# Optimization experiments

Hardware: AMD Instinct MI355X
Metric: run time of the kernel (lower is better)

Reference implementation:

```python
import jax, jax.numpy as jnp
import numpy as np

IN, H, OUT = 8, 256, 24  # input_size, hidden_size, output_size
B, T = 2048, 256


def _gate_step(hx, x, Wx, Wh, b):
    # Fused version of the 8 per-gate Linears: one [.,IN]@[IN,4H] + one [.,H]@[H,4H]
    gates = x @ Wx + hx @ Wh + b            # [B, 4H]
    i, f, o, g = jnp.split(gates, 4, axis=-1)
    i, f, o = jax.nn.sigmoid(i), jax.nn.sigmoid(f), jax.nn.sigmoid(o)
    g = jnp.tanh(g)
    # NOTE: in the original code cx is never reassigned, so it stays zeros and
    # cy = cx*f + i*g == i*g on every step. We replicate that exactly.
    cy = i * g
    return o * jnp.tanh(cy)


def setup_inputs() -> dict:
    key = jax.random.key(0)
    ks = jax.random.split(key, 9)
    s = 0.05
    return {
        "inputs0": jax.random.normal(ks[0], (B, T, IN), jnp.float32),
        "inputs1": jax.random.normal(ks[1], (B, OUT - 1), jnp.float32),
        # concatenated gate weights, order [i | f | o | c]
        "Wx": jax.random.normal(ks[2], (IN, 4 * H), jnp.float32) * s,
        "Wh": jax.random.normal(ks[3], (H, 4 * H), jnp.float32) * s,
        "b": jax.random.normal(ks[4], (4 * H,), jnp.float32) * s,  # bx + bh folded
        "Wy": jax.random.normal(ks[5], (H, 1), jnp.float32) * s,
        "by": jax.random.normal(ks[6], (1,), jnp.float32) * s,
        # fresh random Linear(1, IN) per decoder step in the original -> per-step params
        "dec_w": jax.random.normal(ks[7], (OUT - 1, IN), jnp.float32) * s,
        "dec_b": jax.random.normal(ks[8], (OUT - 1, IN), jnp.float32) * s,
    }


def reference(inputs0, inputs1, Wx, Wh, b, Wy, by, dec_w, dec_b):
    bsz = inputs0.shape[0]
    h0 = jnp.zeros((bsz, H), inputs0.dtype)

    # ---- encoder: scan over time (strict recurrence) ----
    x_seq = jnp.transpose(inputs0, (1, 0, 2))  # [T, B, IN]

    def enc_step(h, x):
        return _gate_step(h, x, Wx, Wh, b), None

    h, _ = jax.lax.scan(enc_step, h0, x_seq)
    hy0 = h @ Wy + by                           # [B, 1]

    # ---- decoder: OUT-1 steps, each with its own fresh 1->IN linear ----
    x1_seq = jnp.transpose(inputs1, (1, 0))[: OUT - 1]  # [OUT-1, B]

    def dec_step(h, inp):
        x1, w, bb = inp
        x = x1[:, None] * w[None, :] + bb[None, :]      # [B, IN]
        h = _gate_step(h, x, Wx, Wh, b)
        return h, h @ Wy + by                            # y: [B, 1]

    _, ys = jax.lax.scan(dec_step, h, (x1_seq, dec_w, dec_b))  # ys: [OUT-1, B, 1]

    hy = jnp.concatenate([hy0, jnp.transpose(ys[..., 0], (1, 0))], axis=1)  # [B, OUT]
    return hy
```

## Files before the change

### kernel.cpp

```cpp
#include <hip/hip_runtime.h>


typedef short bf16x8 __attribute__((ext_vector_type(8)));
typedef float f32x4 __attribute__((ext_vector_type(4)));

#define T_ENC 256
#define N_DEC 23
#define NSTEP 279
#define HSTR 296
#define REG_T 45
#define LDS_T 9
#define WPACK_SHORTS (48 * 9 * 512)

__device__ __forceinline__ short f2bf(float f) {
  unsigned u = __float_as_uint(f);
  u = (u + 0x7fffu + ((u >> 16) & 1u)) >> 16;
  return (short)u;
}
__device__ __forceinline__ float bf2f(short s) {
  return __uint_as_float(((unsigned)(unsigned short)s) << 16);
}

#if __has_builtin(__builtin_amdgcn_rcpf)
#define RCPF(x) __builtin_amdgcn_rcpf(x)
#else
#define RCPF(x) (1.0f / (x))
#endif

__device__ __forceinline__ float sigm(float x) { return RCPF(1.0f + __expf(-x)); }
__device__ __forceinline__ float tanhf_fast(float x) {
  return 1.0f - 2.0f * RCPF(__expf(2.0f * x) + 1.0f);
}

__global__ void pack_kernel(const float* __restrict__ Wx, const float* __restrict__ Wh,
                            const float* __restrict__ b, short* __restrict__ Wpack) {
  int tau = blockIdx.x;
  int l = threadIdx.x;
  int n_tile = tau / 9, kt = tau % 9;
  int w = n_tile / 6, t = n_tile % 6;
  int gate = t >> 1, loc = t & 1;
  int base = (gate == 0) ? 0 : (gate == 1 ? 512 : 768);
  int c = l & 15, q = l >> 4;
  int oc = base + w * 32 + loc * 16 + c;
  bf16x8 v;
#pragma unroll
  for (int e = 0; e < 8; ++e) {
    int k = kt * 32 + q * 8 + e;
    float f;
    if (k < 256)       f = Wh[k * 1024 + oc];
    else if (k < 264)  f = Wx[(k - 256) * 1024 + oc];
    else if (k == 264) f = b[oc];
    else               f = 0.0f;
    v[e] = f2bf(f);
  }
  ((bf16x8*)Wpack)[tau * 64 + l] = v;
}

__global__ __launch_bounds__(512, 2) void lstm_kernel(
    const float* __restrict__ inputs0, const float* __restrict__ inputs1,
    const float* __restrict__ Wy, const float* __restrict__ by,
    const float* __restrict__ dec_w, const float* __restrict__ dec_b,
    const short* __restrict__ Wpack, float* __restrict__ out) {
  __shared__ __align__(16) short B_lds[8 * LDS_T * 512];
  __shared__ __align__(16) short hbuf[16 * HSTR];
  __shared__ float Wy_lds[256];
  __shared__ float ypart[128];

  const int tid = threadIdx.x;
  const int wg = blockIdx.x;
  const int lane = tid & 63;
  const int w = tid >> 6;
  const int q = lane >> 4;
  const int c = lane & 15;

  const bf16x8* wp = (const bf16x8*)Wpack;

  bf16x8 Breg[REG_T];
#pragma unroll
  for (int r = 0; r < REG_T; ++r) Breg[r] = wp[(w * 54 + r) * 64 + lane];
#pragma unroll
  for (int j = 0; j < LDS_T; ++j) {
    bf16x8 v = wp[(w * 54 + REG_T + j) * 64 + lane];
    *(bf16x8*)(B_lds + (w * LDS_T + j) * 512 + lane * 8) = v;
  }

  for (int i = tid; i < 16 * HSTR; i += 512) hbuf[i] = 0;
  if (tid < 256) Wy_lds[tid] = Wy[tid];
  __syncthreads();

  if (tid < 64) {
    int m = tid >> 3, kk = tid & 7;
    hbuf[m * HSTR + 256 + kk] = f2bf(inputs0[((wg * 8 + m) * 256 + 0) * 8 + kk]);
  }
  if (tid < 8) hbuf[tid * HSTR + 264] = (short)0x3F80;
  const float byv = by[0];
  __syncthreads();

#define RDA(kt) (*(const bf16x8*)(hbuf + (c & 7) * HSTR + (kt) * 32 + q * 8))
#define LDSB(j) (*(const bf16x8*)(B_lds + (w * LDS_T + (j)) * 512 + lane * 8))

  for (int s = 0; s < NSTEP; ++s) {
    float xv = 0.0f;
    const bool do_x = (tid < 64) && (s + 1 < NSTEP);
    const int xm = tid >> 3, xk = tid & 7;
    if (do_x) {
      int sn = s + 1;
      if (sn < T_ENC) {
        xv = inputs0[((wg * 8 + xm) * 256 + sn) * 8 + xk];
      } else {
        int d = sn - T_ENC;
        xv = inputs1[(wg * 8 + xm) * N_DEC + d] * dec_w[d * 8 + xk] + dec_b[d * 8 + xk];
      }
    }

    bf16x8 A3[3];
    A3[0] = RDA(0); A3[1] = RDA(1); A3[2] = RDA(2);
    f32x4 acc[6];
#pragma unroll
    for (int t = 0; t < 6; ++t) { acc[t][0] = 0.f; acc[t][1] = 0.f; acc[t][2] = 0.f; acc[t][3] = 0.f; }
#pragma unroll
    for (int kt = 0; kt < 9; ++kt) {
      const bf16x8 a = A3[kt % 3];
#pragma unroll
      for (int t = 0; t < 5; ++t)
        acc[t] = __builtin_amdgcn_mfma_f32_16x16x32_bf16(a, Breg[t * 9 + kt], acc[t], 0, 0, 0);
      acc[5] = __builtin_amdgcn_mfma_f32_16x16x32_bf16(a, LDSB(kt), acc[5], 0, 0, 0);
      if (kt + 3 < 9) A3[kt % 3] = RDA(kt + 3);
    }
    __syncthreads();

    const int qh = q >> 1;
    const f32x4 vi = qh ? acc[1] : acc[0];
    const f32x4 vo = qh ? acc[3] : acc[2];
    const f32x4 vg = qh ? acc[5] : acc[4];
    const int row0 = (q & 1) * 4;
    const int colw = w * 32 + qh * 16 + c;
#pragma unroll
    for (int j = 0; j < 4; ++j) {
      float ii = sigm(vi[j]);
      float oo = sigm(vo[j]);
      float gg = tanhf_fast(vg[j]);
      float h = oo * tanhf_fast(ii * gg);
      hbuf[(row0 + j) * HSTR + colw] = f2bf(h);
    }
    if (do_x) hbuf[xm * HSTR + 256 + xk] = f2bf(xv);
    __syncthreads();

    if (s >= T_ENC - 1) {
      if (tid < 128) {
        int m = tid & 7, kq = tid >> 3;
        const short* hp = hbuf + m * HSTR + kq * 16;
        bf16x8 h0 = *(const bf16x8*)(hp);
        bf16x8 h1 = *(const bf16x8*)(hp + 8);
        float part = 0.0f;
#pragma unroll
        for (int j = 0; j < 8; ++j) {
          part += bf2f(h0[j]) * Wy_lds[kq * 16 + j];
          part += bf2f(h1[j]) * Wy_lds[kq * 16 + 8 + j];
        }
        ypart[tid] = part;
      }
      __syncthreads();
      if (tid < 8) {
        float y = byv;
#pragma unroll
        for (int kq = 0; kq < 16; ++kq) y += ypart[kq * 8 + tid];
        out[(wg * 8 + tid) * 24 + (s - (T_ENC - 1))] = y;
      }
    }
  }
}

extern "C" void kernel_launch(void* const* d_in, const int* in_sizes, int n_in,
                              void* d_out, int out_size, void* d_ws, size_t ws_size,
                              hipStream_t stream) {
  const float* inputs0 = (const float*)d_in[0];
  const float* inputs1 = (const float*)d_in[1];
  const float* Wx      = (const float*)d_in[2];
  const float* Wh      = (const float*)d_in[3];
  const float* b       = (const float*)d_in[4];
  const float* Wy      = (const float*)d_in[5];
  const float* by      = (const float*)d_in[6];
  const float* dec_w   = (const float*)d_in[7];
  const float* dec_b   = (const float*)d_in[8];

  short* Wpack = (short*)d_ws;

  pack_kernel<<<dim3(48 * 9), dim3(64), 0, stream>>>(Wx, Wh, b, Wpack);
  lstm_kernel<<<dim3(256), dim3(512), 0, stream>>>(
      inputs0, inputs1, Wy, by, dec_w, dec_b, Wpack, (float*)d_out);
}
```

Baseline: 425.0 us.

## Split hidden units across workgroup pairs with global-memory h exchange

Each pair of workgroups now handles 16 batch rows, and each workgroup computes half of the hidden units, so it holds 27 weight fragments in registers instead of spilling part of the weights to LDS. Each step, a workgroup publishes its half of h to global memory, sets a step flag, spin-waits on the partner's flag, and copies the partner's half into a double-buffered LDS h buffer. The aim is fewer MFMAs per wave and no weight reads from LDS, with 16-row tiles filling the MFMA M dimension. The cost is a cross-workgroup handshake through global memory on every one of the 279 steps. This relies on both partners being co-resident, which the large dynamic LDS request is meant to enforce, and otherwise risks deadlock.

```diff
diff --git a/kernel.cpp b/kernel.cpp
--- a/kernel.cpp
+++ b/kernel.cpp
@@ -8,9 +8,8 @@
 #define N_DEC 23
 #define NSTEP 279
 #define HSTR 296
-#define REG_T 45
-#define LDS_T 9
-#define WPACK_SHORTS (48 * 9 * 512)
+#define X_OFF 458752
+#define FLAG_OFF (X_OFF + 128 * 2 * 2 * 4096)
 
 __device__ __forceinline__ short f2bf(float f) {
   unsigned u = __float_as_uint(f);
@@ -37,11 +36,11 @@
   int tau = blockIdx.x;
   int l = threadIdx.x;
   int n_tile = tau / 9, kt = tau % 9;
-  int w = n_tile / 6, t = n_tile % 6;
-  int gate = t >> 1, loc = t & 1;
-  int base = (gate == 0) ? 0 : (gate == 1 ? 512 : 768);
+  int eta = n_tile / 24, rem = n_tile % 24;
+  int w = rem / 3, t = rem % 3;
+  int base = (t == 0) ? 0 : (t == 1 ? 512 : 768);
   int c = l & 15, q = l >> 4;
-  int oc = base + w * 32 + loc * 16 + c;
+  int oc = base + eta * 128 + w * 16 + c;
   bf16x8 v;
 #pragma unroll
   for (int e = 0; e < 8; ++e) {
@@ -56,18 +55,27 @@
   ((bf16x8*)Wpack)[tau * 64 + l] = v;
 }
 
+__global__ void init_flags(unsigned* __restrict__ flags) {
+  int i = blockIdx.x * 256 + threadIdx.x;
+  if (i < 4096) flags[i] = 0u;
+}
+
 __global__ __launch_bounds__(512, 2) void lstm_kernel(
     const float* __restrict__ inputs0, const float* __restrict__ inputs1,
     const float* __restrict__ Wy, const float* __restrict__ by,
     const float* __restrict__ dec_w, const float* __restrict__ dec_b,
-    const short* __restrict__ Wpack, float* __restrict__ out) {
-  __shared__ __align__(16) short B_lds[8 * LDS_T * 512];
-  __shared__ __align__(16) short hbuf[16 * HSTR];
+    const short* __restrict__ Wpack, unsigned long long* __restrict__ Xall,
+    unsigned* __restrict__ flags, float* __restrict__ out) {
+  __shared__ __align__(16) short hbuf[2][16 * HSTR];
   __shared__ float Wy_lds[256];
-  __shared__ float ypart[128];
+  __shared__ float ypart[256];
+  extern __shared__ char lds_pad[];
 
   const int tid = threadIdx.x;
   const int wg = blockIdx.x;
+  const int eta = (wg >> 3) & 1;
+  const int etap = eta ^ 1;
+  const int P = ((wg >> 4) << 3) | (wg & 7);
   const int lane = tid & 63;
   const int w = tid >> 6;
   const int q = lane >> 4;
@@ -75,81 +83,107 @@
 
   const bf16x8* wp = (const bf16x8*)Wpack;
 
-  bf16x8 Breg[REG_T];
-#pragma unroll
-  for (int r = 0; r < REG_T; ++r) Breg[r] = wp[(w * 54 + r) * 64 + lane];
-#pragma unroll
-  for (int j = 0; j < LDS_T; ++j) {
-    bf16x8 v = wp[(w * 54 + REG_T + j) * 64 + lane];
-    *(bf16x8*)(B_lds + (w * LDS_T + j) * 512 + lane * 8) = v;
-  }
-
-  for (int i = tid; i < 16 * HSTR; i += 512) hbuf[i] = 0;
+  bf16x8 Breg[27];
+#pragma unroll
+  for (int r = 0; r < 27; ++r)
+    Breg[r] = wp[((eta * 8 + w) * 27 + r) * 64 + lane];
+
+  unsigned* flagOwn = flags + (P * 2 + eta) * 16;
+  unsigned* flagPar = flags + (P * 2 + etap) * 16;
+
+  for (int i = tid; i < 2 * 16 * HSTR; i += 512) hbuf[0][i] = 0;
   if (tid < 256) Wy_lds[tid] = Wy[tid];
   __syncthreads();
-
-  if (tid < 64) {
+  if (tid < 128) {
     int m = tid >> 3, kk = tid & 7;
-    hbuf[m * HSTR + 256 + kk] = f2bf(inputs0[((wg * 8 + m) * 256 + 0) * 8 + kk]);
+    hbuf[0][m * HSTR + 256 + kk] = f2bf(inputs0[((P * 16 + m) * 256 + 0) * 8 + kk]);
   }
-  if (tid < 8) hbuf[tid * HSTR + 264] = (short)0x3F80;
+  if (tid < 32) hbuf[tid >> 4][(tid & 15) * HSTR + 264] = (short)0x3F80;
   const float byv = by[0];
+  const int hcol = eta * 128 + w * 16 + c;
   __syncthreads();
 
-#define RDA(kt) (*(const bf16x8*)(hbuf + (c & 7) * HSTR + (kt) * 32 + q * 8))
-#define LDSB(j) (*(const bf16x8*)(B_lds + (w * LDS_T + (j)) * 512 + lane * 8))
-
   for (int s = 0; s < NSTEP; ++s) {
+    const int cur = s & 1, nxt = cur ^ 1;
+    const short* hc = &hbuf[cur][0];
+    short* hn = &hbuf[nxt][0];
+
     float xv = 0.0f;
-    const bool do_x = (tid < 64) && (s + 1 < NSTEP);
+    const bool do_x = (tid < 128) && (s + 1 < NSTEP);
     const int xm = tid >> 3, xk = tid & 7;
     if (do_x) {
       int sn = s + 1;
       if (sn < T_ENC) {
-        xv = inputs0[((wg * 8 + xm) * 256 + sn) * 8 + xk];
+        xv = inputs0[((P * 16 + xm) * 256 + sn) * 8 + xk];
       } else {
         int d = sn - T_ENC;
-        xv = inputs1[(wg * 8 + xm) * N_DEC + d] * dec_w[d * 8 + xk] + dec_b[d * 8 + xk];
-      }
-    }
-
-    bf16x8 A3[3];
-    A3[0] = RDA(0); A3[1] = RDA(1); A3[2] = RDA(2);
-    f32x4 acc[6];
-#pragma unroll
-    for (int t = 0; t < 6; ++t) { acc[t][0] = 0.f; acc[t][1] = 0.f; acc[t][2] = 0.f; acc[t][3] = 0.f; }
+        xv = inputs1[(P * 16 + xm) * N_DEC + d] * dec_w[d * 8 + xk] + dec_b[d * 8 + xk];
+      }
+    }
+
+    bf16x8 A[9];
+#pragma unroll
+    for (int kt = 0; kt < 9; ++kt)
+      A[kt] = *(const bf16x8*)(hc + c * HSTR + kt * 32 + q * 8);
+
+    f32x4 acc[3];
+#pragma unroll
+    for (int t = 0; t < 3; ++t) { acc[t][0] = 0.f; acc[t][1] = 0.f; acc[t][2] = 0.f; acc[t][3] = 0.f; }
+    __builtin_amdgcn_s_setprio(1);
 #pragma unroll
     for (int kt = 0; kt < 9; ++kt) {
-      const bf16x8 a = A3[kt % 3];
-#pragma unroll
-      for (int t = 0; t < 5; ++t)
-        acc[t] = __builtin_amdgcn_mfma_f32_16x16x32_bf16(a, Breg[t * 9 + kt], acc[t], 0, 0, 0);
-      acc[5] = __builtin_amdgcn_mfma_f32_16x16x32_bf16(a, LDSB(kt), acc[5], 0, 0, 0);
-      if (kt + 3 < 9) A3[kt % 3] = RDA(kt + 3);
-    }
+#pragma unroll
+      for (int t = 0; t < 3; ++t)
+        acc[t] = __builtin_amdgcn_mfma_f32_16x16x32_bf16(A[kt], Breg[t * 9 + kt], acc[t], 0, 0, 0);
+    }
+    __builtin_amdgcn_s_setprio(0);
+
+    short hb[4];
+#pragma unroll
+    for (int r = 0; r < 4; ++r) {
+      float ii = sigm(acc[0][r]);
+      float oo = sigm(acc[1][r]);
+      float gg = tanhf_fast(acc[2][r]);
+      hb[r] = f2bf(oo * tanhf_fast(ii * gg));
+      hn[(4 * q + r) * HSTR + hcol] = hb[r];
+    }
+    unsigned long long pk =
+        (unsigned long long)(unsigned short)hb[0] |
+        ((unsigned long long)(unsigned short)hb[1] << 16) |
+        ((unsigned long long)(unsigned short)hb[2] << 32) |
+        ((unsigned long long)(unsigned short)hb[3] << 48);
+    unsigned long long* Xown = Xall + ((unsigned)(P * 2 + nxt) * 2 + eta) * 512;
+    __hip_atomic_store(&Xown[(w * 16 + c) * 4 + q], pk,
+                       __ATOMIC_RELAXED, __HIP_MEMORY_SCOPE_AGENT);
+    if (do_x) hn[xm * HSTR + 256 + xk] = f2bf(xv);
     __syncthreads();
 
-    const int qh = q >> 1;
-    const f32x4 vi = qh ? acc[1] : acc[0];
-    const f32x4 vo = qh ? acc[3] : acc[2];
-    const f32x4 vg = qh ? acc[5] : acc[4];
-    const int row0 = (q & 1) * 4;
-    const int colw = w * 32 + qh * 16 + c;
-#pragma unroll
-    for (int j = 0; j < 4; ++j) {
-      float ii = sigm(vi[j]);
-      float oo = sigm(vo[j]);
-      float gg = tanhf_fast(vg[j]);
-      float h = oo * tanhf_fast(ii * gg);
-      hbuf[(row0 + j) * HSTR + colw] = f2bf(h);
-    }
-    if (do_x) hbuf[xm * HSTR + 256 + xk] = f2bf(xv);
+    if (tid == 0)
+      __hip_atomic_store(&flagOwn[nxt], (unsigned)(s + 1),
+                         __ATOMIC_RELAXED, __HIP_MEMORY_SCOPE_AGENT);
+    {
+      const unsigned want = (unsigned)(s + 1);
+      unsigned v = __hip_atomic_load(&flagPar[nxt], __ATOMIC_RELAXED, __HIP_MEMORY_SCOPE_AGENT);
+      while (v != want) {
+        __builtin_amdgcn_s_sleep(2);
+        v = __hip_atomic_load(&flagPar[nxt], __ATOMIC_RELAXED, __HIP_MEMORY_SCOPE_AGENT);
+      }
+    }
+    {
+      unsigned long long* Xpar = Xall + ((unsigned)(P * 2 + nxt) * 2 + etap) * 512;
+      unsigned long long pk2 = __hip_atomic_load(&Xpar[tid], __ATOMIC_RELAXED, __HIP_MEMORY_SCOPE_AGENT);
+      int col = tid >> 2, rg = tid & 3;
+      int pcol = etap * 128 + col;
+#pragma unroll
+      for (int j = 0; j < 4; ++j)
+        hn[(4 * rg + j) * HSTR + pcol] = (short)(pk2 >> (16 * j));
+    }
     __syncthreads();
 
-    if (s >= T_ENC - 1) {
-      if (tid < 128) {
-        int m = tid & 7, kq = tid >> 3;
-        const short* hp = hbuf + m * HSTR + kq * 16;
+    if (eta == 0 && s >= T_ENC - 1) {
+      if (tid < 256) {
+        int m = tid & 15, kq = tid >> 4;
+        const short* hp = hn + m * HSTR + kq * 16;
         bf16x8 h0 = *(const bf16x8*)(hp);
         bf16x8 h1 = *(const bf16x8*)(hp + 8);
         float part = 0.0f;
@@ -161,11 +195,11 @@
         ypart[tid] = part;
       }
       __syncthreads();
-      if (tid < 8) {
+      if (tid < 16) {
         float y = byv;
 #pragma unroll
-        for (int kq = 0; kq < 16; ++kq) y += ypart[kq * 8 + tid];
-        out[(wg * 8 + tid) * 24 + (s - (T_ENC - 1))] = y;
+        for (int kq = 0; kq < 16; ++kq) y += ypart[kq * 16 + tid];
+        out[(P * 16 + tid) * 24 + (s - (T_ENC - 1))] = y;
       }
     }
   }
@@ -185,8 +219,11 @@
   const float* dec_b   = (const float*)d_in[8];
 
   short* Wpack = (short*)d_ws;
-
-  pack_kernel<<<dim3(48 * 9), dim3(64), 0, stream>>>(Wx, Wh, b, Wpack);
-  lstm_kernel<<<dim3(256), dim3(512), 0, stream>>>(
-      inputs0, inputs1, Wy, by, dec_w, dec_b, Wpack, (float*)d_out);
-}
+  unsigned long long* Xall = (unsigned long long*)((char*)d_ws + X_OFF);
+  unsigned* flags = (unsigned*)((char*)d_ws + FLAG_OFF);
+
+  pack_kernel<<<dim3(432), dim3(64), 0, stream>>>(Wx, Wh, b, Wpack);
+  init_flags<<<dim3(16), dim3(256), 0, stream>>>(flags);
+  lstm_kernel<<<dim3(256), dim3(512), 65536, stream>>>(
+      inputs0, inputs1, Wy, by, dec_w, dec_b, Wpack, Xall, flags, (float*)d_out);
+}
```

Result: slower. 611.6 us (+43.9%).
